# Optimization experiments

Measured on AMD Instinct MI355X. Metric: run time of the kernel, lower is better.

The kernel has to match this reference:

```python
import jax, jax.numpy as jnp
import numpy as np

NC = 6            # CPAB tessellation cells (tess_size=6, zero_boundary=True)
DIM = NC - 1      # theta dimension = 5
SIG_LEN = 2048
CHANNELS = 3
BATCH = 256
FC_IN = 64 * 168  # flattened net_part1 output for signal_len=2048
NUM_SCALING = 0   # N in transform_data_ss
EPS_BN = 1e-5


def _cpab_basis():
    """QR null-space basis of the CPAB continuity + zero-boundary constraints.
    Params ordered [a_1,b_1,...,a_NC,b_NC]; v(x)=a_c x + b_c on cell c."""
    nc = NC
    L = np.zeros((nc + 1, 2 * nc))
    for k in range(1, nc):  # continuity at internal knots x_k = k/nc
        xk = k / nc
        L[k - 1, 2 * (k - 1)] = xk
        L[k - 1, 2 * (k - 1) + 1] = 1.0
        L[k - 1, 2 * k] = -xk
        L[k - 1, 2 * k + 1] = -1.0
    L[nc - 1, 1] = 1.0        # v(0) = 0  -> b_1 = 0
    L[nc, 2 * (nc - 1)] = 1.0  # v(1) = 0 -> a_nc + b_nc = 0
    L[nc, 2 * nc - 1] = 1.0
    Q, _ = np.linalg.qr(L.T, mode='complete')
    return np.ascontiguousarray(Q[:, nc + 1:]).astype(np.float32)  # (12, 5)


def _conv1d(x, w, b):
    y = jax.lax.conv_general_dilated(x, w, (1,), 'VALID',
                                     dimension_numbers=('NCH', 'OIH', 'NCH'))
    return y + b[None, :, None]


def _maxpool1d(x, k, s):
    return jax.lax.reduce_window(x, -jnp.inf, jax.lax.max, (1, 1, k), (1, 1, s), 'VALID')


def _bn(x, g, b, m, v):  # eval-mode BatchNorm1d
    return (x - m[None, :, None]) * (g / jnp.sqrt(v + EPS_BN))[None, :, None] + b[None, :, None]


def _integrate(x, A):
    """Exact CPAB 1D flow integration over t=1 with cell-crossing handling.
    x: (B, n) points in [0,1]; A: (B, NC, 2) per-cell (a, b). Monotone
    trajectories cross at most NC-1 boundaries -> fixed NC+1 iterations."""
    a_all, b_all = A[:, :, 0], A[:, :, 1]
    t = jnp.ones_like(x)
    for _ in range(NC + 1):
        c = jnp.clip(jnp.floor(x * NC).astype(jnp.int32), 0, NC - 1)
        a = jnp.take_along_axis(a_all, c, axis=1)
        b = jnp.take_along_axis(b_all, c, axis=1)
        v = a * x + b
        xb = jnp.where(v >= 0, (c + 1).astype(x.dtype) / NC, c.astype(x.dtype) / NC)
        big_a = jnp.abs(a) > 1e-8
        a_s = jnp.where(big_a, a, 1.0)
        z = x + b / a_s        # shifted coord: x(t) = z*exp(a t) - b/a
        zb = xb + b / a_s
        ratio = zb / jnp.where(jnp.abs(z) > 1e-12, z, 1e-12)
        t_exp = jnp.log(jnp.maximum(ratio, 1e-12)) / a_s
        v_s = jnp.where(jnp.abs(v) > 1e-12, v, 1.0)
        t_lin = (xb - x) / v_s
        thit = jnp.where(big_a, t_exp, t_lin)
        valid = (jnp.abs(v) > 1e-12) & (thit > 0) & (jnp.where(big_a, ratio, 1.0) > 0)
        thit = jnp.where(valid, thit, jnp.inf)
        tau = jnp.minimum(t, thit)
        x_new = jnp.where(big_a, z * jnp.exp(a * tau) - (z - x), x + b * tau)
        hit = thit <= t
        nudge = jnp.where(v >= 0, 1e-6, -1e-6)  # push into next cell
        x = jnp.clip(jnp.where(hit, xb + nudge, x_new), 0.0, 1.0)
        t = jnp.maximum(t - tau, 0.0)
    return x


def _interp1d(data, pos):
    """data: (B, L, C); pos: (B, n) in [0,1] -> (B, n, C) linear interpolation."""
    Lw = data.shape[1]
    p = jnp.clip(pos, 0.0, 1.0) * (Lw - 1)
    x0 = jnp.clip(jnp.floor(p).astype(jnp.int32), 0, Lw - 2)
    w = (p - x0.astype(p.dtype))[:, :, None]
    d0 = jnp.take_along_axis(data, x0[:, :, None], axis=1)
    d1 = jnp.take_along_axis(data, (x0 + 1)[:, :, None], axis=1)
    return d0 * (1.0 - w) + d1 * w


def _transform_data_ss(data, theta, basis, outsize, N):
    """CPAB scaling-and-squaring warp of data (B, L, C) by theta (B, DIM)."""
    Bsz = theta.shape[0]
    A = (theta @ basis.T).reshape(Bsz, NC, 2) / (2.0 ** N)
    grid = jnp.linspace(0.0, 1.0, outsize, dtype=data.dtype)
    grid_t = _integrate(jnp.broadcast_to(grid, (Bsz, outsize)), A)
    for _ in range(N):  # squaring: compose the warp with itself
        grid_t = _interp1d(grid_t[:, :, None], grid_t)[:, :, 0]
    return _interp1d(data, grid_t)


def reference(x, conv1_w, conv1_b, bn1_g, bn1_b, bn1_m, bn1_v,
              conv2_w, conv2_b, bn2_g, bn2_b, bn2_m, bn2_v,
              conv3_w, conv3_b, bn3_g, bn3_b, bn3_m, bn3_v,
              fc1_w, fc1_b, fc2_w, fc2_b, fc3_w, fc3_b, fc4_w, fc4_b, basis):
    # localization net (n_recurrence = 1, back_version = True)
    h = jax.nn.relu(_maxpool1d(_bn(_conv1d(x, conv1_w, conv1_b), bn1_g, bn1_b, bn1_m, bn1_v), 3, 2))
    h = jax.nn.relu(_maxpool1d(_bn(_conv1d(h, conv2_w, conv2_b), bn2_g, bn2_b, bn2_m, bn2_v), 3, 3))
    h = jax.nn.relu(_maxpool1d(_bn(_conv1d(h, conv3_w, conv3_b), bn3_g, bn3_b, bn3_m, bn3_v), 3, 2))
    xs = h.reshape(h.shape[0], -1)  # (B, 64*168)
    xs = jax.nn.relu(xs @ fc1_w.T + fc1_b)
    xs = jax.nn.relu(xs @ fc2_w.T + fc2_b)
    xs = jax.nn.relu(xs @ fc3_w.T + fc3_b)
    theta = jnp.tanh(xs @ fc4_w.T + fc4_b)  # (B, 5)
    data = jnp.transpose(x, (0, 2, 1))       # (B, L, C)
    warped = _transform_data_ss(data, theta, basis, SIG_LEN, NUM_SCALING)
    return jnp.transpose(warped, (0, 2, 1))  # (B, C, L)


def setup_inputs() -> dict:
    key = jax.random.key(0)
    ks = jax.random.split(key, 16)
    def nrm(k, shape, scale):
        return (jax.random.normal(k, shape) * scale).astype(jnp.float32)
    inp = {}
    inp['x'] = jax.random.normal(ks[0], (BATCH, CHANNELS, SIG_LEN), dtype=jnp.float32)
    inp['conv1_w'] = nrm(ks[1], (128, CHANNELS, 3), (CHANNELS * 3) ** -0.5)
    inp['conv1_b'] = nrm(ks[2], (128,), 0.01)
    inp['bn1_g'] = jnp.ones((128,), jnp.float32)
    inp['bn1_b'] = jnp.zeros((128,), jnp.float32)
    inp['bn1_m'] = nrm(ks[3], (128,), 0.1)
    inp['bn1_v'] = jnp.ones((128,), jnp.float32)
    inp['conv2_w'] = nrm(ks[4], (64, 128, 5), (128 * 5) ** -0.5)
    inp['conv2_b'] = nrm(ks[5], (64,), 0.01)
    inp['bn2_g'] = jnp.ones((64,), jnp.float32)
    inp['bn2_b'] = jnp.zeros((64,), jnp.float32)
    inp['bn2_m'] = nrm(ks[6], (64,), 0.1)
    inp['bn2_v'] = jnp.ones((64,), jnp.float32)
    inp['conv3_w'] = nrm(ks[7], (64, 64, 3), (64 * 3) ** -0.5)
    inp['conv3_b'] = nrm(ks[8], (64,), 0.01)
    inp['bn3_g'] = jnp.ones((64,), jnp.float32)
    inp['bn3_b'] = jnp.zeros((64,), jnp.float32)
    inp['bn3_m'] = nrm(ks[9], (64,), 0.1)
    inp['bn3_v'] = jnp.ones((64,), jnp.float32)
    inp['fc1_w'] = nrm(ks[10], (48, FC_IN), FC_IN ** -0.5)
    inp['fc1_b'] = jnp.zeros((48,), jnp.float32)
    inp['fc2_w'] = nrm(ks[11], (32, 48), 48 ** -0.5)
    inp['fc2_b'] = jnp.zeros((32,), jnp.float32)
    inp['fc3_w'] = nrm(ks[12], (16, 32), 32 ** -0.5)
    inp['fc3_b'] = jnp.zeros((16,), jnp.float32)
    # near-identity warp head (original zero-inits weight, identity bias)
    inp['fc4_w'] = nrm(ks[13], (DIM, 16), 0.01)
    inp['fc4_b'] = nrm(ks[14], (DIM,), 0.01)
    inp['basis'] = jnp.asarray(_cpab_basis())
    return inp
```

## Files before the change

kernel.cpp:

```cpp
#include <hip/hip_runtime.h>
#include <math.h>

#define BATCH   256
#define SIGLEN  2048
#define L1OUT   1022
#define L2OUT   339
#define L3OUT   168
#define FCIN    10752

#define TP2   16
#define NROW  52
#define H1S   136
#define H1SZ  (NROW*H1S)

#define H3R   346

typedef float f32x2  __attribute__((ext_vector_type(2)));
typedef float f32x4  __attribute__((ext_vector_type(4)));
typedef short s16x8  __attribute__((ext_vector_type(8)));

__device__ __forceinline__ unsigned short f2bf(float f) {
    unsigned int u = __float_as_uint(f);
    return (unsigned short)((u + 0x7fffu + ((u >> 16) & 1u)) >> 16);
}
__device__ __forceinline__ float bf2f(unsigned short h) {
    return __uint_as_float(((unsigned int)h) << 16);
}
__device__ __forceinline__ f32x2 pkfma(f32x2 a, f32x2 b, f32x2 c) {
    f32x2 d;
    asm("v_pk_fma_f32 %0, %1, %2, %3" : "=v"(d) : "v"(a), "v"(b), "v"(c));
    return d;
}

__launch_bounds__(256)
__global__ void prep_kernel(
    const float* __restrict__ conv1_b,
    const float* __restrict__ g1, const float* __restrict__ b1,
    const float* __restrict__ m1, const float* __restrict__ v1,
    const float* __restrict__ conv2_w, const float* __restrict__ conv2_b,
    const float* __restrict__ g2, const float* __restrict__ b2,
    const float* __restrict__ m2, const float* __restrict__ v2,
    const float* __restrict__ conv3_w, const float* __restrict__ conv3_b,
    const float* __restrict__ g3, const float* __restrict__ b3,
    const float* __restrict__ m3, const float* __restrict__ v3,
    const float* __restrict__ fc1_w,
    unsigned short* __restrict__ w2hi, unsigned short* __restrict__ w2lo,
    unsigned short* __restrict__ w3hi, unsigned short* __restrict__ w3lo,
    float* __restrict__ wp1,
    float* __restrict__ so1, float* __restrict__ so2, float* __restrict__ so3)
{
    __shared__ float tl[64 * 169];

    int t   = threadIdx.x;
    int tid = blockIdx.x * 256 + t;
    int stride = gridDim.x * 256;

    if (blockIdx.x < 48) {
        int o = blockIdx.x;
        for (int i = t; i < FCIN; i += 256) {
            int co = i / L3OUT, u = i - co * L3OUT;
            tl[co * 169 + u] = fc1_w[o * FCIN + i];
        }
        __syncthreads();
        for (int i = t; i < FCIN; i += 256) {
            int u = i >> 6, co = i & 63;
            wp1[o * FCIN + i] = tl[co * 169 + u];
        }
    }

    for (int i = tid; i < 64*128*5; i += stride) {
        int co = i / 640; int rr = i - co*640; int ci = rr / 5; int k = rr - ci*5;
        float w = conv2_w[i];
        unsigned short hi = f2bf(w);
        unsigned short lo = f2bf(w - bf2f(hi));
        int dst = ((k*4 + (ci >> 5))*64 + co)*32 + (ci & 31);
        w2hi[dst] = hi;
        w2lo[dst] = lo;
    }
    for (int i = tid; i < 64*64*3; i += stride) {
        int co = i / 192; int r = i - co*192; int ci = r / 3; int k = r - ci*3;
        float w = conv3_w[i];
        unsigned short hi = f2bf(w);
        unsigned short lo = f2bf(w - bf2f(hi));
        int dst = ((k*2 + (ci >> 5))*64 + co)*32 + (ci & 31);
        w3hi[dst] = hi;
        w3lo[dst] = lo;
    }
    if (tid < 128) {
        float s = g1[tid] / sqrtf(v1[tid] + 1e-5f);
        so1[tid]       = s;
        so1[128 + tid] = (conv1_b[tid] - m1[tid]) * s + b1[tid];
    }
    if (tid < 64) {
        float s2 = g2[tid] / sqrtf(v2[tid] + 1e-5f);
        so2[tid]      = s2;
        so2[64 + tid] = (conv2_b[tid] - m2[tid]) * s2 + b2[tid];
        float s3 = g3[tid] / sqrtf(v3[tid] + 1e-5f);
        so3[tid]      = s3;
        so3[64 + tid] = (conv3_b[tid] - m3[tid]) * s3 + b3[tid];
    }
}

__launch_bounds__(256, 5)
__global__ void conv12_kernel(
    const float* __restrict__ x, const float* __restrict__ w1,
    const unsigned short* __restrict__ w2hi, const unsigned short* __restrict__ w2lo,
    const float* __restrict__ so1, const float* __restrict__ so2,
    unsigned int* __restrict__ h2p)
{
    __shared__ unsigned short h1hi[H1SZ];
    __shared__ unsigned short h1lo[H1SZ];

    int t  = threadIdx.x;
    int b  = blockIdx.x;
    int u0 = blockIdx.y * TP2;
    int q0 = 3 * u0;
    int wv = __builtin_amdgcn_readfirstlane(t >> 6);
    int l  = t & 63;
    int m  = l & 15;
    int qd = l >> 4;

    {
        f32x2 wp[9], s1p, o1p;
        const float* wa = w1 + (2*l)*9;
        #pragma unroll
        for (int j = 0; j < 9; ++j) wp[j] = (f32x2){wa[j], wa[9 + j]};
        s1p = (f32x2){so1[2*l], so1[2*l + 1]};
        o1p = (f32x2){so1[128 + 2*l], so1[128 + 2*l + 1]};

        int rbase = 13 * wv;
        int W0 = 2*(q0 + rbase);
        const float* xp0 = x + b*3*SIGLEN;

        f32x2 xb[3][6];
        if (W0 + 5 <= SIGLEN - 1) {
            #pragma unroll
            for (int ci = 0; ci < 3; ++ci) {
                const float* xp = xp0 + ci*SIGLEN + W0;
                float2 v01 = *(const float2*)(xp);
                float2 v23 = *(const float2*)(xp + 2);
                float2 v45 = *(const float2*)(xp + 4);
                xb[ci][0] = (f32x2){v01.x, v01.x};
                xb[ci][1] = (f32x2){v01.y, v01.y};
                xb[ci][2] = (f32x2){v23.x, v23.x};
                xb[ci][3] = (f32x2){v23.y, v23.y};
                xb[ci][4] = (f32x2){v45.x, v45.x};
                xb[ci][5] = (f32x2){v45.y, v45.y};
            }
        } else {
            #pragma unroll
            for (int ci = 0; ci < 3; ++ci)
                #pragma unroll
                for (int j = 0; j < 6; ++j) {
                    int xi = W0 + j; xi = xi < SIGLEN ? xi : SIGLEN - 1;
                    float v = xp0[ci*SIGLEN + xi];
                    xb[ci][j] = (f32x2){v, v};
                }
        }

        f32x2 cr = (f32x2){0.f, 0.f};
        #pragma unroll
        for (int s = 0; s < 13; ++s) {
            int r = rbase + s;
            f32x2 r1 = (f32x2){0.f, 0.f}, r2 = (f32x2){0.f, 0.f};
            #pragma unroll
            for (int ci = 0; ci < 3; ++ci) {
                #pragma unroll
                for (int tp = 0; tp < 3; ++tp) {
                    r1 = pkfma(xb[ci][1 + tp], wp[ci*3 + tp], r1);
                    r2 = pkfma(xb[ci][2 + tp], wp[ci*3 + tp], r2);
                }
            }
            f32x2 r0;
            if (s == 0) {
                r0 = (f32x2){0.f, 0.f};
                #pragma unroll
                for (int ci = 0; ci < 3; ++ci)
                    #pragma unroll
                    for (int tp = 0; tp < 3; ++tp)
                        r0 = pkfma(xb[ci][tp], wp[ci*3 + tp], r0);
            } else {
                r0 = cr;
            }
            cr = r2;

            float m0 = fmaxf(r0[0], fmaxf(r1[0], r2[0]));
            float m1 = fmaxf(r0[1], fmaxf(r1[1], r2[1]));
            float v0 = fmaxf(fmaf(s1p[0], m0, o1p[0]), 0.f);
            float v1 = fmaxf(fmaf(s1p[1], m1, o1p[1]), 0.f);

            unsigned ua = __float_as_uint(v0);
            unsigned ub = __float_as_uint(v1);
            unsigned hipack = __builtin_amdgcn_perm(ub, ua, 0x07060302u);
            float ra = v0 - __uint_as_float(ua & 0xffff0000u);
            float rb = v1 - __uint_as_float(ub & 0xffff0000u);
            unsigned lopack = __builtin_amdgcn_perm(__float_as_uint(rb), __float_as_uint(ra),
                                                    0x07060302u);
            ((unsigned*)h1hi)[r*68 + l] = hipack;
            ((unsigned*)h1lo)[r*68 + l] = lopack;

            if (s < 12) {
                #pragma unroll
                for (int ci = 0; ci < 3; ++ci) {
                    xb[ci][0] = xb[ci][2]; xb[ci][1] = xb[ci][3];
                    xb[ci][2] = xb[ci][4]; xb[ci][3] = xb[ci][5];
                }
                int Wn = W0 + 2*s + 6;
                if (Wn + 1 <= SIGLEN - 1) {
                    #pragma unroll
                    for (int ci = 0; ci < 3; ++ci) {
                        float2 v = *(const float2*)(xp0 + ci*SIGLEN + Wn);
                        xb[ci][4] = (f32x2){v.x, v.x};
                        xb[ci][5] = (f32x2){v.y, v.y};
                    }
                } else {
                    #pragma unroll
                    for (int ci = 0; ci < 3; ++ci) {
                        int x4 = Wn     < SIGLEN ? Wn     : SIGLEN - 1;
                        int x5 = Wn + 1 < SIGLEN ? Wn + 1 : SIGLEN - 1;
                        float a4 = xp0[ci*SIGLEN + x4];
                        float a5 = xp0[ci*SIGLEN + x5];
                        xb[ci][4] = (f32x2){a4, a4};
                        xb[ci][5] = (f32x2){a5, a5};
                    }
                }
            }
        }
    }
    __syncthreads();

    f32x4 acc[3] = {(f32x4)(0.f), (f32x4)(0.f), (f32x4)(0.f)};

    const unsigned short* whb = w2hi + wv*512 + m*32 + qd*8;
    const unsigned short* wlb = w2lo + wv*512 + m*32 + qd*8;

    for (int k = 0; k < 5; ++k) {
        #pragma unroll
        for (int cb = 0; cb < 4; ++cb) {
            int st = k*4 + cb;
            s16x8 wh = *(const s16x8*)(whb + st*2048);
            s16x8 wl = *(const s16x8*)(wlb + st*2048);
            #pragma unroll
            for (int pt = 0; pt < 3; ++pt) {
                int row = pt*16 + m + k;
                s16x8 ah = *(const s16x8*)&h1hi[row*H1S + cb*32 + qd*8];
                s16x8 al = *(const s16x8*)&h1lo[row*H1S + cb*32 + qd*8];
                acc[pt] = __builtin_amdgcn_mfma_f32_16x16x32_bf16(ah, wh, acc[pt], 0, 0, 0);
                acc[pt] = __builtin_amdgcn_mfma_f32_16x16x32_bf16(al, wh, acc[pt], 0, 0, 0);
                acc[pt] = __builtin_amdgcn_mfma_f32_16x16x32_bf16(ah, wl, acc[pt], 0, 0, 0);
            }
        }
    }
    __syncthreads();

    float* c2 = (float*)h1hi;
    #pragma unroll
    for (int pt = 0; pt < 3; ++pt)
        #pragma unroll
        for (int rg = 0; rg < 4; ++rg)
            c2[(pt*16 + qd*4 + rg)*65 + wv*16 + m] = acc[pt][rg];
    __syncthreads();

    #pragma unroll
    for (int it = 0; it < 4; ++it) {
        int idx = t + it*256;
        int ul = idx >> 6, co = idx & 63;
        int u = u0 + ul;
        if (u < L2OUT) {
            float v0 = c2[(3*ul  )*65 + co];
            float v1 = c2[(3*ul+1)*65 + co];
            float v2 = c2[(3*ul+2)*65 + co];
            float mm = fmaxf(v0, fmaxf(v1, v2));
            float v  = fmaxf(fmaf(so2[co], mm, so2[64 + co]), 0.f);
            unsigned uu = __float_as_uint(v);
            float rr = v - __uint_as_float(uu & 0xffff0000u);
            h2p[(b*L2OUT + u)*64 + co] = (uu >> 16) | (__float_as_uint(rr) & 0xffff0000u);
        }
    }
}

__launch_bounds__(1024, 1)
__global__ void tail_kernel(
    const unsigned int* __restrict__ h2p,
    const unsigned short* __restrict__ w3hi, const unsigned short* __restrict__ w3lo,
    const float* __restrict__ so3, const float* __restrict__ wp1,
    const float* __restrict__ fc1_b,
    const float* __restrict__ fc2_w, const float* __restrict__ fc2_b,
    const float* __restrict__ fc3_w, const float* __restrict__ fc3_b,
    const float* __restrict__ fc4_w, const float* __restrict__ fc4_b,
    const float* __restrict__ basis,
    const float* __restrict__ x,
    float* __restrict__ out)
{
    __shared__ unsigned short h3s[2*H3R*72];
    __shared__ float c3buf[64*65];
    __shared__ float xsr[48];
    __shared__ float xs48[48], hl[32], gl[16], thl[5], Al[12];

    int t  = threadIdx.x;
    int b  = blockIdx.x;
    int wv = __builtin_amdgcn_readfirstlane(t >> 6);
    int l  = t & 63;
    int m  = l & 15;
    int qd = l >> 4;
    int pt = wv >> 2;
    int c4 = wv & 3;

    {
        const unsigned int* src = h2p + (b*L2OUT)*64;
        unsigned* dhi = (unsigned*)h3s;
        unsigned* dlo = (unsigned*)(h3s + H3R*72);
        for (int i = t; i < H3R*32; i += 1024) {
            int r = i >> 5, cp = i & 31;
            int g = r > (L2OUT-1) ? (L2OUT-1) : r;
            uint2 v = ((const uint2*)src)[g*32 + cp];
            dhi[r*36 + cp] = __builtin_amdgcn_perm(v.y, v.x, 0x05040100u);
            dlo[r*36 + cp] = __builtin_amdgcn_perm(v.y, v.x, 0x07060302u);
        }
    }

    s16x8 wh[6], wl[6];
    #pragma unroll
    for (int s = 0; s < 6; ++s) {
        wh[s] = *(const s16x8*)(w3hi + s*2048 + (c4*16 + m)*32 + qd*8);
        wl[s] = *(const s16x8*)(w3lo + s*2048 + (c4*16 + m)*32 + qd*8);
    }
    float s3 = so3[l], o3 = so3[64 + l];

    __syncthreads();

    int o0 = wv * 3;
    float fa[3] = {0.f, 0.f, 0.f};

    for (int ti = 0; ti < 6; ++ti) {
        int u0 = ti * 28;

        f32x4 acc = (f32x4)(0.f);
        #pragma unroll
        for (int s = 0; s < 6; ++s) {
            int row = 2*u0 + pt*16 + m + (s >> 1);
            int off = (s & 1)*32 + qd*8;
            s16x8 ah = *(const s16x8*)&h3s[row*72 + off];
            s16x8 al = *(const s16x8*)&h3s[H3R*72 + row*72 + off];
            acc = __builtin_amdgcn_mfma_f32_16x16x32_bf16(ah, wh[s], acc, 0, 0, 0);
            acc = __builtin_amdgcn_mfma_f32_16x16x32_bf16(al, wh[s], acc, 0, 0, 0);
            acc = __builtin_amdgcn_mfma_f32_16x16x32_bf16(ah, wl[s], acc, 0, 0, 0);
        }
        __syncthreads();

        #pragma unroll
        for (int rg = 0; rg < 4; ++rg)
            c3buf[(pt*16 + qd*4 + rg)*65 + c4*16 + m] = acc[rg];
        __syncthreads();

        #pragma unroll 4
        for (int u = 0; u < 28; ++u) {
            int p = 2*u;
            float v0 = c3buf[(p  )*65 + l];
            float v1 = c3buf[(p+1)*65 + l];
            float v2 = c3buf[(p+2)*65 + l];
            float pv = fmaxf(fmaf(s3, fmaxf(v0, fmaxf(v1, v2)), o3), 0.f);
            const float* wp = wp1 + (u0 + u)*64 + l;
            #pragma unroll
            for (int j = 0; j < 3; ++j)
                fa[j] = fmaf(pv, wp[(o0 + j)*FCIN], fa[j]);
        }
    }

    #pragma unroll
    for (int j = 0; j < 3; ++j) {
        #pragma unroll
        for (int off = 32; off > 0; off >>= 1)
            fa[j] += __shfl_xor(fa[j], off, 64);
    }
    if (l == 0) {
        #pragma unroll
        for (int j = 0; j < 3; ++j) xsr[o0 + j] = fa[j];
    }
    __syncthreads();

    if (t < 48) xs48[t] = fmaxf(xsr[t] + fc1_b[t], 0.f);
    __syncthreads();
    if (t < 32) {
        float sv = fc2_b[t];
        #pragma unroll
        for (int k = 0; k < 48; ++k) sv = fmaf(fc2_w[t * 48 + k], xs48[k], sv);
        hl[t] = fmaxf(sv, 0.f);
    }
    __syncthreads();
    if (t < 16) {
        float sv = fc3_b[t];
        #pragma unroll
        for (int k = 0; k < 32; ++k) sv = fmaf(fc3_w[t * 32 + k], hl[k], sv);
        gl[t] = fmaxf(sv, 0.f);
    }
    __syncthreads();
    if (t < 5) {
        float sv = fc4_b[t];
        #pragma unroll
        for (int k = 0; k < 16; ++k) sv = fmaf(fc4_w[t * 16 + k], gl[k], sv);
        thl[t] = tanhf(sv);
    }
    __syncthreads();
    if (t < 12) {
        float sv = 0.f;
        #pragma unroll
        for (int d = 0; d < 5; ++d) sv = fmaf(basis[t * 5 + d], thl[d], sv);
        Al[t] = sv;
    }
    __syncthreads();

    float a_r[6], b_r[6];
    #pragma unroll
    for (int c = 0; c < 6; ++c) { a_r[c] = Al[2*c]; b_r[c] = Al[2*c+1]; }

    #pragma unroll
    for (int cc = 0; cc < 2; ++cc) {
        int i = cc * 1024 + t;
        float xp = (float)i / 2047.f;
        float tt = 1.f;
        for (int it = 0; it < 7; ++it) {
            int c = (int)floorf(xp * 6.f);
            c = min(max(c, 0), 5);
            float a  = a_r[c], bb = b_r[c];
            float v  = a * xp + bb;
            float xb = (v >= 0.f) ? (float)(c + 1) / 6.f : (float)c / 6.f;
            bool  big_a = fabsf(a) > 1e-8f;
            float a_s = big_a ? a : 1.f;
            float z   = xp + bb / a_s;
            float zb  = xb + bb / a_s;
            float zden = (fabsf(z) > 1e-12f) ? z : 1e-12f;
            float ratio = zb / zden;
            float t_exp = logf(fmaxf(ratio, 1e-12f)) / a_s;
            float v_s   = (fabsf(v) > 1e-12f) ? v : 1.f;
            float t_lin = (xb - xp) / v_s;
            float thit  = big_a ? t_exp : t_lin;
            bool valid  = (fabsf(v) > 1e-12f) && (thit > 0.f) && ((big_a ? ratio : 1.f) > 0.f);
            if (!valid) thit = __builtin_inff();
            float tau   = fminf(tt, thit);
            float x_new = big_a ? (z * expf(a * tau) - (z - xp)) : (xp + bb * tau);
            bool hit    = (thit <= tt);
            float nudge = (v >= 0.f) ? 1e-6f : -1e-6f;
            xp = hit ? (xb + nudge) : x_new;
            xp = fminf(fmaxf(xp, 0.f), 1.f);
            tt = fmaxf(tt - tau, 0.f);
        }
        float p = fminf(fmaxf(xp, 0.f), 1.f) * 2047.f;
        int i0 = (int)floorf(p);
        i0 = min(max(i0, 0), 2046);
        float w = p - (float)i0;
        #pragma unroll
        for (int c = 0; c < 3; ++c) {
            const float* d = &x[(b * 3 + c) * SIGLEN];
            out[(b * 3 + c) * SIGLEN + i] = d[i0] * (1.f - w) + d[i0 + 1] * w;
        }
    }
}

extern "C" void kernel_launch(void* const* d_in, const int* in_sizes, int n_in,
                              void* d_out, int out_size, void* d_ws, size_t ws_size,
                              hipStream_t stream) {
    (void)in_sizes; (void)n_in; (void)out_size; (void)ws_size;
    const float* x       = (const float*)d_in[0];
    const float* conv1_w = (const float*)d_in[1];
    const float* conv1_b = (const float*)d_in[2];
    const float* bn1_g   = (const float*)d_in[3];
    const float* bn1_b   = (const float*)d_in[4];
    const float* bn1_m   = (const float*)d_in[5];
    const float* bn1_v   = (const float*)d_in[6];
    const float* conv2_w = (const float*)d_in[7];
    const float* conv2_b = (const float*)d_in[8];
    const float* bn2_g   = (const float*)d_in[9];
    const float* bn2_b   = (const float*)d_in[10];
    const float* bn2_m   = (const float*)d_in[11];
    const float* bn2_v   = (const float*)d_in[12];
    const float* conv3_w = (const float*)d_in[13];
    const float* conv3_b = (const float*)d_in[14];
    const float* bn3_g   = (const float*)d_in[15];
    const float* bn3_b   = (const float*)d_in[16];
    const float* bn3_m   = (const float*)d_in[17];
    const float* bn3_v   = (const float*)d_in[18];
    const float* fc1_w   = (const float*)d_in[19];
    const float* fc1_b   = (const float*)d_in[20];
    const float* fc2_w   = (const float*)d_in[21];
    const float* fc2_b   = (const float*)d_in[22];
    const float* fc3_w   = (const float*)d_in[23];
    const float* fc3_b   = (const float*)d_in[24];
    const float* fc4_w   = (const float*)d_in[25];
    const float* fc4_b   = (const float*)d_in[26];
    const float* basis   = (const float*)d_in[27];

    unsigned short* w2hi = (unsigned short*)d_ws;
    unsigned short* w2lo = w2hi + 40960;
    unsigned short* w3hi = w2lo + 40960;
    unsigned short* w3lo = w3hi + 12288;
    float* ws   = (float*)d_ws;
    float* so1  = ws + 53248;
    float* so2  = so1 + 256;
    float* so3  = so2 + 128;
    float* wp1  = so3 + 128;
    unsigned int* h2p = (unsigned int*)(wp1 + 516096);

    prep_kernel<<<128, 256, 0, stream>>>(
        conv1_b, bn1_g, bn1_b, bn1_m, bn1_v,
        conv2_w, conv2_b, bn2_g, bn2_b, bn2_m, bn2_v,
        conv3_w, conv3_b, bn3_g, bn3_b, bn3_m, bn3_v,
        fc1_w, w2hi, w2lo, w3hi, w3lo, wp1, so1, so2, so3);

    dim3 g2(BATCH, (L2OUT + TP2 - 1) / TP2);
    conv12_kernel<<<g2, 256, 0, stream>>>(x, conv1_w, w2hi, w2lo, so1, so2, h2p);

    tail_kernel<<<BATCH, 1024, 0, stream>>>(h2p, w3hi, w3lo, so3, wp1,
                                            fc1_b, fc2_w, fc2_b, fc3_w, fc3_b,
                                            fc4_w, fc4_b, basis, x, (float*)d_out);
}
```

Measured before the change: 238.4 us.

## Vectorize fc1 weight transpose, spread prep work across blocks, vectorize tail fc1 dot

The prep kernel now uses float4 loads and stores for the fc1 weight transpose and gives each conv2/conv3/BN element its own thread across a larger grid (512 blocks) instead of grid-stride loops. In the tail kernel, pooling plus BN+ReLU is computed once per element into a shared buffer. The fc1 dot product then reads float4 chunks of pooled values and weights, replacing scalar strided weight loads. This is meant to cut global-load instruction count and latency, at the cost of an extra barrier and shared memory per tile.

```diff
diff --git a/kernel.cpp b/kernel.cpp
--- a/kernel.cpp
+++ b/kernel.cpp
@@ -53,51 +53,69 @@
 
     int t   = threadIdx.x;
     int tid = blockIdx.x * 256 + t;
-    int stride = gridDim.x * 256;
 
     if (blockIdx.x < 48) {
         int o = blockIdx.x;
-        for (int i = t; i < FCIN; i += 256) {
-            int co = i / L3OUT, u = i - co * L3OUT;
-            tl[co * 169 + u] = fc1_w[o * FCIN + i];
+        for (int i4 = 4*t; i4 < FCIN; i4 += 1024) {
+            int co = i4 / L3OUT, u = i4 - co * L3OUT;
+            float4 v = *(const float4*)(fc1_w + o*FCIN + i4);
+            tl[co*169 + u    ] = v.x;
+            tl[co*169 + u + 1] = v.y;
+            tl[co*169 + u + 2] = v.z;
+            tl[co*169 + u + 3] = v.w;
         }
         __syncthreads();
-        for (int i = t; i < FCIN; i += 256) {
-            int u = i >> 6, co = i & 63;
-            wp1[o * FCIN + i] = tl[co * 169 + u];
-        }
-    }
-
-    for (int i = tid; i < 64*128*5; i += stride) {
-        int co = i / 640; int rr = i - co*640; int ci = rr / 5; int k = rr - ci*5;
-        float w = conv2_w[i];
-        unsigned short hi = f2bf(w);
-        unsigned short lo = f2bf(w - bf2f(hi));
-        int dst = ((k*4 + (ci >> 5))*64 + co)*32 + (ci & 31);
-        w2hi[dst] = hi;
-        w2lo[dst] = lo;
-    }
-    for (int i = tid; i < 64*64*3; i += stride) {
-        int co = i / 192; int r = i - co*192; int ci = r / 3; int k = r - ci*3;
-        float w = conv3_w[i];
-        unsigned short hi = f2bf(w);
-        unsigned short lo = f2bf(w - bf2f(hi));
-        int dst = ((k*2 + (ci >> 5))*64 + co)*32 + (ci & 31);
-        w3hi[dst] = hi;
-        w3lo[dst] = lo;
-    }
-    if (tid < 128) {
-        float s = g1[tid] / sqrtf(v1[tid] + 1e-5f);
-        so1[tid]       = s;
-        so1[128 + tid] = (conv1_b[tid] - m1[tid]) * s + b1[tid];
-    }
-    if (tid < 64) {
-        float s2 = g2[tid] / sqrtf(v2[tid] + 1e-5f);
-        so2[tid]      = s2;
-        so2[64 + tid] = (conv2_b[tid] - m2[tid]) * s2 + b2[tid];
-        float s3 = g3[tid] / sqrtf(v3[tid] + 1e-5f);
-        so3[tid]      = s3;
-        so3[64 + tid] = (conv3_b[tid] - m3[tid]) * s3 + b3[tid];
+        for (int i4 = 4*t; i4 < FCIN; i4 += 1024) {
+            int u = i4 >> 6, co = i4 & 63;
+            float4 v;
+            v.x = tl[(co    )*169 + u];
+            v.y = tl[(co + 1)*169 + u];
+            v.z = tl[(co + 2)*169 + u];
+            v.w = tl[(co + 3)*169 + u];
+            *(float4*)(wp1 + o*FCIN + i4) = v;
+        }
+    }
+
+    {
+        int i = tid - 16384;
+        if ((unsigned)i < 40960u) {
+            int co = i / 640; int rr = i - co*640; int ci = rr / 5; int k = rr - ci*5;
+            float w = conv2_w[i];
+            unsigned short hi = f2bf(w);
+            unsigned short lo = f2bf(w - bf2f(hi));
+            int dst = ((k*4 + (ci >> 5))*64 + co)*32 + (ci & 31);
+            w2hi[dst] = hi;
+            w2lo[dst] = lo;
+        }
+    }
+    {
+        int i = tid - 57344;
+        if ((unsigned)i < 12288u) {
+            int co = i / 192; int r = i - co*192; int ci = r / 3; int k = r - ci*3;
+            float w = conv3_w[i];
+            unsigned short hi = f2bf(w);
+            unsigned short lo = f2bf(w - bf2f(hi));
+            int dst = ((k*2 + (ci >> 5))*64 + co)*32 + (ci & 31);
+            w3hi[dst] = hi;
+            w3lo[dst] = lo;
+        }
+    }
+    {
+        int i = tid - 69632;
+        if ((unsigned)i < 128u) {
+            float s = g1[i] / sqrtf(v1[i] + 1e-5f);
+            so1[i]       = s;
+            so1[128 + i] = (conv1_b[i] - m1[i]) * s + b1[i];
+        }
+        int i2 = tid - 69888;
+        if ((unsigned)i2 < 64u) {
+            float s2 = g2[i2] / sqrtf(v2[i2] + 1e-5f);
+            so2[i2]      = s2;
+            so2[64 + i2] = (conv2_b[i2] - m2[i2]) * s2 + b2[i2];
+            float s3 = g3[i2] / sqrtf(v3[i2] + 1e-5f);
+            so3[i2]      = s3;
+            so3[64 + i2] = (conv3_b[i2] - m3[i2]) * s3 + b3[i2];
+        }
     }
 }
 
@@ -294,6 +312,7 @@
 {
     __shared__ unsigned short h3s[2*H3R*72];
     __shared__ float c3buf[64*65];
+    __shared__ float pools[28*64];
     __shared__ float xsr[48];
     __shared__ float xs48[48], hl[32], gl[16], thl[5], Al[12];
 
@@ -325,11 +344,12 @@
         wh[s] = *(const s16x8*)(w3hi + s*2048 + (c4*16 + m)*32 + qd*8);
         wl[s] = *(const s16x8*)(w3lo + s*2048 + (c4*16 + m)*32 + qd*8);
     }
-    float s3 = so3[l], o3 = so3[64 + l];
 
     __syncthreads();
 
     int o0 = wv * 3;
+    int ug  = l >> 4;
+    int co4 = (l & 15) * 4;
     float fa[3] = {0.f, 0.f, 0.f};
 
     for (int ti = 0; ti < 6; ++ti) {
@@ -353,17 +373,30 @@
             c3buf[(pt*16 + qd*4 + rg)*65 + c4*16 + m] = acc[rg];
         __syncthreads();
 
-        #pragma unroll 4
-        for (int u = 0; u < 28; ++u) {
-            int p = 2*u;
-            float v0 = c3buf[(p  )*65 + l];
-            float v1 = c3buf[(p+1)*65 + l];
-            float v2 = c3buf[(p+2)*65 + l];
-            float pv = fmaxf(fmaf(s3, fmaxf(v0, fmaxf(v1, v2)), o3), 0.f);
-            const float* wp = wp1 + (u0 + u)*64 + l;
+        #pragma unroll
+        for (int k = 0; k < 2; ++k) {
+            int idx = t + k*1024;
+            if (idx < 28*64) {
+                int u = idx >> 6, co = idx & 63;
+                int p = 2*u;
+                float v0 = c3buf[(p  )*65 + co];
+                float v1 = c3buf[(p+1)*65 + co];
+                float v2 = c3buf[(p+2)*65 + co];
+                pools[idx] = fmaxf(fmaf(so3[co], fmaxf(v0, fmaxf(v1, v2)), so3[64 + co]), 0.f);
+            }
+        }
+        __syncthreads();
+
+        #pragma unroll
+        for (int uu = 0; uu < 7; ++uu) {
+            int u = 4*uu + ug;
+            f32x4 p = *(const f32x4*)&pools[u*64 + co4];
+            const float* wb = wp1 + (u0 + u)*64 + co4;
             #pragma unroll
-            for (int j = 0; j < 3; ++j)
-                fa[j] = fmaf(pv, wp[(o0 + j)*FCIN], fa[j]);
+            for (int j = 0; j < 3; ++j) {
+                f32x4 w = *(const f32x4*)(wb + (o0 + j)*FCIN);
+                fa[j] = fmaf(p[0], w[0], fmaf(p[1], w[1], fmaf(p[2], w[2], fmaf(p[3], w[3], fa[j]))));
+            }
         }
     }
 
@@ -501,7 +534,7 @@
     float* wp1  = so3 + 128;
     unsigned int* h2p = (unsigned int*)(wp1 + 516096);
 
-    prep_kernel<<<128, 256, 0, stream>>>(
+    prep_kernel<<<512, 256, 0, stream>>>(
         conv1_b, bn1_g, bn1_b, bn1_m, bn1_v,
         conv2_w, conv2_b, bn2_g, bn2_b, bn2_m, bn2_v,
         conv3_w, conv3_b, bn3_g, bn3_b, bn3_m, bn3_v,
```

New measurement: 245.1 us. 2.8% more time.
